# Optimization experiments

Measured on AMD Instinct MI355X. Metric: run time of the kernel, lower is better.

The kernel has to match this reference:

```python
import jax, jax.numpy as jnp
import numpy as np


def _proj_prelu(x, W, b, a):
    # 1x1 conv (pointwise linear over channels) + PReLU with scalar slope
    y = jnp.einsum('nchw,oc->nohw', x, W) + b[None, :, None, None]
    return jnp.where(y >= 0, y, a[0] * y)


def setup_inputs() -> dict:
    key = jax.random.key(0)
    ks = jax.random.split(key, 8)
    C, Ce = 128, 64
    x = jax.random.normal(ks[0], (4, C, 80, 80), dtype=jnp.float32)
    s = 1.0 / np.sqrt(C)
    Wq = jax.random.normal(ks[1], (Ce, C), dtype=jnp.float32) * s
    bq = jax.random.normal(ks[2], (Ce,), dtype=jnp.float32) * 0.01
    Wk = jax.random.normal(ks[3], (Ce, C), dtype=jnp.float32) * s
    bk = jax.random.normal(ks[4], (Ce,), dtype=jnp.float32) * 0.01
    Wv = jax.random.normal(ks[5], (C, C), dtype=jnp.float32) * s
    bv = jax.random.normal(ks[6], (C,), dtype=jnp.float32) * 0.01
    aq = jnp.full((1,), 0.25, dtype=jnp.float32)
    ak = jnp.full((1,), 0.25, dtype=jnp.float32)
    av = jnp.full((1,), 0.25, dtype=jnp.float32)
    return {'x': x, 'Wq': Wq, 'bq': bq, 'aq': aq, 'Wk': Wk, 'bk': bk,
            'ak': ak, 'Wv': Wv, 'bv': bv, 'av': av}


def reference(x, Wq, bq, aq, Wk, bk, ak, Wv, bv, av):
    q = _proj_prelu(x, Wq, bq, aq)   # [N, Ce, H, W]
    k = _proj_prelu(x, Wk, bk, ak)   # [N, Ce, H, W]
    v = _proj_prelu(x, Wv, bv, av)   # [N, C,  H, W]
    N, Ce, H, W = q.shape
    Cv = v.shape[1]
    HW = H * W
    qf = q.reshape(N, Ce, HW)        # torch permute+view -> [N, HW, Ce] = qf^T
    kf = k.reshape(N, Ce, HW)
    vf = v.reshape(N, Cv, HW)
    score = jnp.einsum('nci,ncj->nij', qf, kf)      # [N, HW, HW]
    attn = jax.nn.softmax(score, axis=2)
    out = jnp.einsum('nij,ncj->nci', attn, vf)      # [N, Cv, HW]
    return out.reshape(N, Cv, H, W)
```

## Files before the change

kernel.cpp:

```cpp
#include <hip/hip_runtime.h>

typedef __attribute__((ext_vector_type(8)))  short bf16x8;
typedef __attribute__((ext_vector_type(16))) float f32x16;
typedef unsigned int u32;
typedef unsigned short u16;

#define HW 6400
#define L2E 1.44269504088896f
#define DEFER_THR 8.0f

__device__ inline u16 f2bf(float f) {
    u32 u = __builtin_bit_cast(u32, f);
    u32 r = (u + 0x7fffu + ((u >> 16) & 1u)) >> 16;
    return (u16)r;
}
__device__ inline u32 cvt_pk_bf16(float lo, float hi) {
    u32 r;
    asm("v_cvt_pk_bf16_f32 %0, %1, %2" : "=v"(r) : "v"(lo), "v"(hi));
    return r;
}
__device__ inline void gload_lds16(const void* g, void* l) {
    __builtin_amdgcn_global_load_lds(
        (const __attribute__((address_space(1))) u32*)g,
        (__attribute__((address_space(3))) u32*)l, 16, 0, 0);
}

__global__ __launch_bounds__(256) void proj_kernel(
    const float* __restrict__ x,
    const float* __restrict__ Wq, const float* __restrict__ bq, const float* __restrict__ aq,
    const float* __restrict__ Wk, const float* __restrict__ bk, const float* __restrict__ ak,
    const float* __restrict__ Wv, const float* __restrict__ bv, const float* __restrict__ av,
    u16* __restrict__ QTc, u16* __restrict__ KT, u16* __restrict__ Vw)
{
    __shared__ char xs[64 * 272];
    __shared__ char ktr[64 * 144];

    const int tid  = threadIdx.x;
    const int lane = tid & 63;
    const int w    = tid >> 6;
    const int l31  = lane & 31;
    const int h    = lane >> 5;

    const int blk = blockIdx.x;
    const int n   = blk / 100;
    const int pt  = blk - n * 100;
    const int p0  = pt * 64;

    const float* xb = x + (size_t)n * 128 * HW + p0;
    #pragma unroll
    for (int it = 0; it < 8; ++it) {
        int idx = it * 256 + tid;
        int c = idx >> 4, p4 = (idx & 15) * 4;
        float4 d = *(const float4*)(xb + (size_t)c * HW + p4);
        *(u16*)(xs + (p4 + 0) * 272 + c * 2) = f2bf(d.x);
        *(u16*)(xs + (p4 + 1) * 272 + c * 2) = f2bf(d.y);
        *(u16*)(xs + (p4 + 2) * 272 + c * 2) = f2bf(d.z);
        *(u16*)(xs + (p4 + 3) * 272 + c * 2) = f2bf(d.w);
    }
    __syncthreads();

    const float* Wsrc; const float* bsrc; float slope; float osc = 1.0f;
    if (w == 0)      { Wsrc = Wq;                 bsrc = bq;             slope = aq[0]; osc = L2E; }
    else if (w == 1) { Wsrc = Wk;                 bsrc = bk;             slope = ak[0]; }
    else             { Wsrc = Wv + (w-2)*64*128;  bsrc = bv + (w-2)*64;  slope = av[0]; }

    bf16x8 wf[2][8];
    #pragma unroll
    for (int cb = 0; cb < 2; ++cb)
        #pragma unroll
        for (int kc = 0; kc < 8; ++kc) {
            const float* ws = Wsrc + (cb * 32 + l31) * 128 + kc * 16 + h * 8;
            float4 a = *(const float4*)ws;
            float4 b = *(const float4*)(ws + 4);
            union { u32 u[4]; bf16x8 v; } uu;
            uu.u[0] = cvt_pk_bf16(a.x, a.y);
            uu.u[1] = cvt_pk_bf16(a.z, a.w);
            uu.u[2] = cvt_pk_bf16(b.x, b.y);
            uu.u[3] = cvt_pk_bf16(b.z, b.w);
            wf[cb][kc] = uu.v;
        }

    f32x16 acc[2][2] = {};
    #pragma unroll
    for (int kc = 0; kc < 8; ++kc) {
        bf16x8 xb0 = *(const bf16x8*)(xs + (l31)      * 272 + kc * 32 + h * 16);
        bf16x8 xb1 = *(const bf16x8*)(xs + (l31 + 32) * 272 + kc * 32 + h * 16);
        acc[0][0] = __builtin_amdgcn_mfma_f32_32x32x16_bf16(wf[0][kc], xb0, acc[0][0], 0, 0, 0);
        acc[0][1] = __builtin_amdgcn_mfma_f32_32x32x16_bf16(wf[0][kc], xb1, acc[0][1], 0, 0, 0);
        acc[1][0] = __builtin_amdgcn_mfma_f32_32x32x16_bf16(wf[1][kc], xb0, acc[1][0], 0, 0, 0);
        acc[1][1] = __builtin_amdgcn_mfma_f32_32x32x16_bf16(wf[1][kc], xb1, acc[1][1], 0, 0, 0);
    }

    if (w != 1) {
        u16* dst = (w == 0) ? (QTc + (size_t)n * 64 * HW)
                            : (Vw + ((size_t)n * 128 + (size_t)(w - 2) * 64) * HW);
        #pragma unroll
        for (int cb = 0; cb < 2; ++cb)
            #pragma unroll
            for (int pb = 0; pb < 2; ++pb)
                #pragma unroll
                for (int r = 0; r < 16; ++r) {
                    int ch = cb * 32 + (r & 3) + 8 * (r >> 2) + 4 * h;
                    float y = acc[cb][pb][r] + bsrc[ch];
                    y = (y >= 0.f) ? y : slope * y;
                    dst[(size_t)ch * HW + p0 + pb * 32 + l31] = f2bf(y * osc);
                }
    } else {
        #pragma unroll
        for (int cb = 0; cb < 2; ++cb)
            #pragma unroll
            for (int pb = 0; pb < 2; ++pb)
                #pragma unroll
                for (int rp = 0; rp < 8; ++rp) {
                    int r0 = rp * 2;
                    int ch = cb * 32 + (r0 & 3) + 8 * (r0 >> 2) + 4 * h;
                    float y0 = acc[cb][pb][r0]     + bsrc[ch];
                    float y1 = acc[cb][pb][r0 + 1] + bsrc[ch + 1];
                    y0 = (y0 >= 0.f) ? y0 : slope * y0;
                    y1 = (y1 >= 0.f) ? y1 : slope * y1;
                    *(u32*)(ktr + (pb * 32 + l31) * 144 + ch * 2) = cvt_pk_bf16(y0, y1);
                }
        #pragma unroll
        for (int i8 = 0; i8 < 8; ++i8) {
            int p = i8 * 8 + (lane >> 3);
            bf16x8 d = *(const bf16x8*)(ktr + p * 144 + (lane & 7) * 16);
            *(bf16x8*)(KT + ((size_t)n * HW + p0 + p) * 64 + (lane & 7) * 8) = d;
        }
    }
}

__global__ __launch_bounds__(256, 3) void attn_kernel(
    const u16* __restrict__ QTc, const u16* __restrict__ KT, const u16* __restrict__ Vw,
    float* __restrict__ out,
    float* __restrict__ Opart, float* __restrict__ Mpart, float* __restrict__ Lpart,
    int jsplit, int NT)
{
    __shared__ char lds[49152];

    const int tid  = threadIdx.x;
    const int lane = tid & 63;
    const int w    = tid >> 6;
    const int l31  = lane & 31;
    const int h    = lane >> 5;

    const int per_n = 50 * jsplit;
    const int n    = blockIdx.x / per_n;
    const int rem  = blockIdx.x - n * per_n;
    const int it   = rem / jsplit;
    const int js   = rem - it * jsplit;
    const int i0   = it * 128;
    const int jt0  = js * NT;

    const int row = i0 + w * 32 + l31;

    const u16* qb = QTc + (size_t)n * 64 * HW + row;
    bf16x8 qf[4];
    #pragma unroll
    for (int kc = 0; kc < 4; ++kc) {
        union { u16 s[8]; bf16x8 v; } uu;
        #pragma unroll
        for (int e = 0; e < 8; ++e)
            uu.s[e] = qb[(size_t)(kc * 16 + h * 8 + e) * HW];
        qf[kc] = uu.v;
    }

    const char* Kg = (const char*)(KT + (size_t)n * HW * 64);
    const char* Vg = (const char*)(Vw + (size_t)n * 128 * HW);

    auto stage = [&](int buf, int jt) {
        char* B = lds + buf * 24576;
        #pragma unroll
        for (int q = 0; q < 2; ++q) {
            int abase = (2 * w + q) * 1024;
            int a = abase + lane * 16;
            int r = a >> 7;
            gload_lds16(Kg + (size_t)jt * 8192 + (size_t)(a ^ ((r & 7) << 4)), B + abase);
        }
        #pragma unroll
        for (int q = 0; q < 4; ++q) {
            int abase = (4 * w + q) * 1024;
            int a = abase + lane * 16;
            int c = a >> 7, off = a & 127;
            gload_lds16(Vg + (size_t)c * 12800 + (size_t)jt * 128 + (size_t)(off ^ ((c & 7) << 4)),
                        B + 8192 + abase);
        }
    };

    f32x16 o_acc[4] = {};
    float m = -3e38f, lsum = 0.f;

    auto compute = [&](int buf) {
        char* Klds = lds + buf * 24576;
        char* Vlds = Klds + 8192;

        f32x16 s0 = {}, s1 = {};
        #pragma unroll
        for (int kc = 0; kc < 4; ++kc) {
            const int cidx = (2 * kc + h) * 16;
            bf16x8 kf0 = *(const bf16x8*)(Klds + l31 * 128        + (cidx ^ ((l31 & 7) << 4)));
            bf16x8 kf1 = *(const bf16x8*)(Klds + (32 + l31) * 128 + (cidx ^ ((l31 & 7) << 4)));
            s0 = __builtin_amdgcn_mfma_f32_32x32x16_bf16(kf0, qf[kc], s0, 0, 0, 0);
            s1 = __builtin_amdgcn_mfma_f32_32x32x16_bf16(kf1, qf[kc], s1, 0, 0, 0);
        }

        float rmax = s0[0];
        #pragma unroll
        for (int r = 1; r < 16; ++r) rmax = fmaxf(rmax, s0[r]);
        #pragma unroll
        for (int r = 0; r < 16; ++r) rmax = fmaxf(rmax, s1[r]);
        rmax = fmaxf(rmax, __shfl_xor(rmax, 32, 64));

        if (__any(rmax > m + DEFER_THR)) {
            float mnew = fmaxf(m, rmax);
            float alpha = exp2f(m - mnew);
            lsum *= alpha;
            #pragma unroll
            for (int cb = 0; cb < 4; ++cb)
                #pragma unroll
                for (int r = 0; r < 16; ++r) o_acc[cb][r] *= alpha;
            m = mnew;
        }

        float rs = 0.f;
        #pragma unroll
        for (int r = 0; r < 16; ++r) { s0[r] = exp2f(s0[r] - m); rs += s0[r]; }
        #pragma unroll
        for (int r = 0; r < 16; ++r) { s1[r] = exp2f(s1[r] - m); rs += s1[r]; }
        rs += __shfl_xor(rs, 32, 64);
        lsum += rs;

        bf16x8 pf[4];
        #pragma unroll
        for (int kb = 0; kb < 4; ++kb) {
            f32x16 sv = (kb < 2) ? s0 : s1;
            const int b = (kb & 1) * 8;
            u32 w0 = cvt_pk_bf16(sv[b + 0], sv[b + 1]);
            u32 w1 = cvt_pk_bf16(sv[b + 2], sv[b + 3]);
            u32 w2 = cvt_pk_bf16(sv[b + 4], sv[b + 5]);
            u32 w3 = cvt_pk_bf16(sv[b + 6], sv[b + 7]);
            asm("v_permlane32_swap_b32 %0, %1" : "+v"(w0), "+v"(w2));
            asm("v_permlane32_swap_b32 %0, %1" : "+v"(w1), "+v"(w3));
            union { u32 u[4]; bf16x8 v; } uu;
            uu.u[0] = w0; uu.u[1] = w1; uu.u[2] = w2; uu.u[3] = w3;
            pf[kb] = uu.v;
        }

        #pragma unroll
        for (int kb = 0; kb < 4; ++kb) {
            const int jidx = (2 * kb + h) * 16;
            #pragma unroll
            for (int cb = 0; cb < 4; ++cb) {
                const int crow = cb * 32 + l31;
                bf16x8 vf = *(const bf16x8*)(Vlds + crow * 128 + (jidx ^ ((crow & 7) << 4)));
                o_acc[cb] = __builtin_amdgcn_mfma_f32_32x32x16_bf16(vf, pf[kb], o_acc[cb], 0, 0, 0);
            }
        }
    };

    stage(0, jt0);
    __syncthreads();
    int t = 0;
    for (; t + 2 <= NT; t += 2) {
        stage(1, jt0 + t + 1);
        compute(0);
        __syncthreads();
        if (t + 2 < NT) stage(0, jt0 + t + 2);
        compute(1);
        __syncthreads();
    }
    if (t < NT) compute(0);

    if (Opart != nullptr) {
        float* Ob = Opart + (size_t)(js * 4 + n) * 128 * HW + row;
        #pragma unroll
        for (int cb = 0; cb < 4; ++cb)
            #pragma unroll
            for (int r = 0; r < 16; ++r) {
                int c = cb * 32 + (r & 3) + 8 * (r >> 2) + 4 * h;
                Ob[(size_t)c * HW] = o_acc[cb][r];
            }
        if (h == 0) {
            Mpart[(size_t)(js * 4 + n) * HW + row] = m;
            Lpart[(size_t)(js * 4 + n) * HW + row] = lsum;
        }
    } else {
        float inv = 1.f / lsum;
        float* ob = out + (size_t)n * 128 * HW + row;
        #pragma unroll
        for (int cb = 0; cb < 4; ++cb)
            #pragma unroll
            for (int r = 0; r < 16; ++r) {
                int c = cb * 32 + (r & 3) + 8 * (r >> 2) + 4 * h;
                ob[(size_t)c * HW] = o_acc[cb][r] * inv;
            }
    }
}

__global__ __launch_bounds__(256) void combine_kernel(
    const float* __restrict__ Opart, const float* __restrict__ Mpart,
    const float* __restrict__ Lpart, float* __restrict__ out)
{
    const int b = blockIdx.x;
    const int n = b / 100;
    const int rem = b - n * 100;
    const int cq = rem / 25;
    const int ic = rem - cq * 25;
    const int i = ic * 256 + threadIdx.x;

    float mj[4], wj[4];
    #pragma unroll
    for (int js = 0; js < 4; ++js) mj[js] = Mpart[(size_t)(js * 4 + n) * HW + i];
    float M = fmaxf(fmaxf(mj[0], mj[1]), fmaxf(mj[2], mj[3]));
    float L = 0.f;
    #pragma unroll
    for (int js = 0; js < 4; ++js) {
        wj[js] = exp2f(mj[js] - M);
        L += Lpart[(size_t)(js * 4 + n) * HW + i] * wj[js];
    }
    const float inv = 1.f / L;

    for (int c = cq * 32; c < cq * 32 + 32; ++c) {
        float acc = 0.f;
        #pragma unroll
        for (int js = 0; js < 4; ++js)
            acc += Opart[((size_t)(js * 4 + n) * 128 + c) * HW + i] * wj[js];
        out[((size_t)n * 128 + c) * HW + i] = acc * inv;
    }
}

extern "C" void kernel_launch(void* const* d_in, const int* in_sizes, int n_in,
                              void* d_out, int out_size, void* d_ws, size_t ws_size,
                              hipStream_t stream) {
    const float* x  = (const float*)d_in[0];
    const float* Wq = (const float*)d_in[1];
    const float* bq = (const float*)d_in[2];
    const float* aq = (const float*)d_in[3];
    const float* Wk = (const float*)d_in[4];
    const float* bk = (const float*)d_in[5];
    const float* ak = (const float*)d_in[6];
    const float* Wv = (const float*)d_in[7];
    const float* bv = (const float*)d_in[8];
    const float* av = (const float*)d_in[9];

    char* wsp = (char*)d_ws;
    u16* QTc = (u16*)wsp;
    u16* KT  = (u16*)(wsp + 3276800);
    u16* Vw  = (u16*)(wsp + 6553600);
    const size_t base = 13107200;
    float* Opart = (float*)(wsp + base);
    float* Mpart = (float*)(wsp + base + 52428800);
    float* Lpart = (float*)(wsp + base + 52428800 + 409600);
    const size_t need = base + 52428800 + 2 * 409600;

    proj_kernel<<<dim3(400), 256, 0, stream>>>(x, Wq, bq, aq, Wk, bk, ak, Wv, bv, av,
                                               QTc, KT, Vw);

    if (ws_size >= need) {
        attn_kernel<<<dim3(4 * 50 * 4), 256, 0, stream>>>(QTc, KT, Vw, (float*)d_out,
                                                          Opart, Mpart, Lpart, 4, 25);
        combine_kernel<<<dim3(400), 256, 0, stream>>>(Opart, Mpart, Lpart, (float*)d_out);
    } else {
        attn_kernel<<<dim3(200), 256, 0, stream>>>(QTc, KT, Vw, (float*)d_out,
                                                   nullptr, nullptr, nullptr, 1, 100);
    }
}
```

Baseline: 134.1 us.

## Process two query row tiles per wave to reuse K/V fragments, split keys five ways

Each wave now handles 64 query rows (two 32-row tiles) instead of 32, so every K and V fragment read from LDS feeds two MFMAs. This halves LDS traffic per unit of work and improves the MFMA-to-load ratio. The LDS layout changes from XOR-swizzled rows to a chunk-major layout, and the row-sum reduction across half-waves moves to the end of the loop. The key dimension is split up to 5 ways when the workspace allows, to keep enough blocks in flight. The costs are higher register pressure (occupancy hint lowered to 2) and a possible LDS bank-conflict change from the new layout.

```diff
diff --git a/kernel.cpp b/kernel.cpp
--- a/kernel.cpp
+++ b/kernel.cpp
@@ -129,7 +129,7 @@
     }
 }
 
-__global__ __launch_bounds__(256, 3) void attn_kernel(
+__global__ __launch_bounds__(256, 2) void attn_kernel(
     const u16* __restrict__ QTc, const u16* __restrict__ KT, const u16* __restrict__ Vw,
     float* __restrict__ out,
     float* __restrict__ Opart, float* __restrict__ Mpart, float* __restrict__ Lpart,
@@ -143,25 +143,29 @@
     const int l31  = lane & 31;
     const int h    = lane >> 5;
 
-    const int per_n = 50 * jsplit;
+    const int per_n = 25 * jsplit;
     const int n    = blockIdx.x / per_n;
     const int rem  = blockIdx.x - n * per_n;
     const int it   = rem / jsplit;
     const int js   = rem - it * jsplit;
-    const int i0   = it * 128;
+    const int i0   = it * 256;
     const int jt0  = js * NT;
 
-    const int row = i0 + w * 32 + l31;
-
-    const u16* qb = QTc + (size_t)n * 64 * HW + row;
-    bf16x8 qf[4];
+    const int rowA = i0 + w * 64 + l31;
+    const int rowB = rowA + 32;
+
+    const u16* qbA = QTc + (size_t)n * 64 * HW + rowA;
+    bf16x8 qfA[4], qfB[4];
     #pragma unroll
     for (int kc = 0; kc < 4; ++kc) {
-        union { u16 s[8]; bf16x8 v; } uu;
-        #pragma unroll
-        for (int e = 0; e < 8; ++e)
-            uu.s[e] = qb[(size_t)(kc * 16 + h * 8 + e) * HW];
-        qf[kc] = uu.v;
+        union { u16 s[8]; bf16x8 v; } ua, ub;
+        #pragma unroll
+        for (int e = 0; e < 8; ++e) {
+            size_t off = (size_t)(kc * 16 + h * 8 + e) * HW;
+            ua.s[e] = qbA[off];
+            ub.s[e] = qbA[off + 32];
+        }
+        qfA[kc] = ua.v; qfB[kc] = ub.v;
     }
 
     const char* Kg = (const char*)(KT + (size_t)n * HW * 64);
@@ -171,88 +175,103 @@
         char* B = lds + buf * 24576;
         #pragma unroll
         for (int q = 0; q < 2; ++q) {
-            int abase = (2 * w + q) * 1024;
-            int a = abase + lane * 16;
-            int r = a >> 7;
-            gload_lds16(Kg + (size_t)jt * 8192 + (size_t)(a ^ ((r & 7) << 4)), B + abase);
+            int cc = w + 4 * q;
+            gload_lds16(Kg + (size_t)jt * 8192 + lane * 128 + cc * 16, B + cc * 1024);
         }
         #pragma unroll
         for (int q = 0; q < 4; ++q) {
-            int abase = (4 * w + q) * 1024;
-            int a = abase + lane * 16;
-            int c = a >> 7, off = a & 127;
-            gload_lds16(Vg + (size_t)c * 12800 + (size_t)jt * 128 + (size_t)(off ^ ((c & 7) << 4)),
-                        B + 8192 + abase);
+            int v = w + 4 * q;
+            int jcc = v >> 1, chalf = v & 1;
+            gload_lds16(Vg + (size_t)(chalf * 64 + lane) * 12800 + (size_t)jt * 128 + jcc * 16,
+                        B + 8192 + v * 1024);
         }
     };
 
-    f32x16 o_acc[4] = {};
-    float m = -3e38f, lsum = 0.f;
+    f32x16 accA[4] = {}, accB[4] = {};
+    float mA = -3e38f, mB = -3e38f, lsA = 0.f, lsB = 0.f;
 
     auto compute = [&](int buf) {
         char* Klds = lds + buf * 24576;
         char* Vlds = Klds + 8192;
 
-        f32x16 s0 = {}, s1 = {};
-        #pragma unroll
-        for (int kc = 0; kc < 4; ++kc) {
-            const int cidx = (2 * kc + h) * 16;
-            bf16x8 kf0 = *(const bf16x8*)(Klds + l31 * 128        + (cidx ^ ((l31 & 7) << 4)));
-            bf16x8 kf1 = *(const bf16x8*)(Klds + (32 + l31) * 128 + (cidx ^ ((l31 & 7) << 4)));
-            s0 = __builtin_amdgcn_mfma_f32_32x32x16_bf16(kf0, qf[kc], s0, 0, 0, 0);
-            s1 = __builtin_amdgcn_mfma_f32_32x32x16_bf16(kf1, qf[kc], s1, 0, 0, 0);
-        }
-
-        float rmax = s0[0];
-        #pragma unroll
-        for (int r = 1; r < 16; ++r) rmax = fmaxf(rmax, s0[r]);
-        #pragma unroll
-        for (int r = 0; r < 16; ++r) rmax = fmaxf(rmax, s1[r]);
-        rmax = fmaxf(rmax, __shfl_xor(rmax, 32, 64));
-
-        if (__any(rmax > m + DEFER_THR)) {
-            float mnew = fmaxf(m, rmax);
-            float alpha = exp2f(m - mnew);
-            lsum *= alpha;
-            #pragma unroll
-            for (int cb = 0; cb < 4; ++cb)
+        #pragma unroll
+        for (int jb = 0; jb < 2; ++jb) {
+            bf16x8 kf[4];
+            #pragma unroll
+            for (int kc = 0; kc < 4; ++kc)
+                kf[kc] = *(const bf16x8*)(Klds + (2 * kc + h) * 1024 + (jb * 32 + l31) * 16);
+
+            f32x16 sA = {}, sB = {};
+            #pragma unroll
+            for (int kc = 0; kc < 4; ++kc) {
+                sA = __builtin_amdgcn_mfma_f32_32x32x16_bf16(kf[kc], qfA[kc], sA, 0, 0, 0);
+                sB = __builtin_amdgcn_mfma_f32_32x32x16_bf16(kf[kc], qfB[kc], sB, 0, 0, 0);
+            }
+
+            float rmxA = sA[0], rmxB = sB[0];
+            #pragma unroll
+            for (int r = 1; r < 16; ++r) {
+                rmxA = fmaxf(rmxA, sA[r]);
+                rmxB = fmaxf(rmxB, sB[r]);
+            }
+            rmxA = fmaxf(rmxA, __shfl_xor(rmxA, 32, 64));
+            rmxB = fmaxf(rmxB, __shfl_xor(rmxB, 32, 64));
+
+            if (__any(rmxA > mA + DEFER_THR) || __any(rmxB > mB + DEFER_THR)) {
+                float mnA = fmaxf(mA, rmxA), mnB = fmaxf(mB, rmxB);
+                float aA = exp2f(mA - mnA), aB = exp2f(mB - mnB);
+                lsA *= aA; lsB *= aB;
                 #pragma unroll
-                for (int r = 0; r < 16; ++r) o_acc[cb][r] *= alpha;
-            m = mnew;
-        }
-
-        float rs = 0.f;
-        #pragma unroll
-        for (int r = 0; r < 16; ++r) { s0[r] = exp2f(s0[r] - m); rs += s0[r]; }
-        #pragma unroll
-        for (int r = 0; r < 16; ++r) { s1[r] = exp2f(s1[r] - m); rs += s1[r]; }
-        rs += __shfl_xor(rs, 32, 64);
-        lsum += rs;
-
-        bf16x8 pf[4];
-        #pragma unroll
-        for (int kb = 0; kb < 4; ++kb) {
-            f32x16 sv = (kb < 2) ? s0 : s1;
-            const int b = (kb & 1) * 8;
-            u32 w0 = cvt_pk_bf16(sv[b + 0], sv[b + 1]);
-            u32 w1 = cvt_pk_bf16(sv[b + 2], sv[b + 3]);
-            u32 w2 = cvt_pk_bf16(sv[b + 4], sv[b + 5]);
-            u32 w3 = cvt_pk_bf16(sv[b + 6], sv[b + 7]);
-            asm("v_permlane32_swap_b32 %0, %1" : "+v"(w0), "+v"(w2));
-            asm("v_permlane32_swap_b32 %0, %1" : "+v"(w1), "+v"(w3));
-            union { u32 u[4]; bf16x8 v; } uu;
-            uu.u[0] = w0; uu.u[1] = w1; uu.u[2] = w2; uu.u[3] = w3;
-            pf[kb] = uu.v;
-        }
-
-        #pragma unroll
-        for (int kb = 0; kb < 4; ++kb) {
-            const int jidx = (2 * kb + h) * 16;
-            #pragma unroll
-            for (int cb = 0; cb < 4; ++cb) {
-                const int crow = cb * 32 + l31;
-                bf16x8 vf = *(const bf16x8*)(Vlds + crow * 128 + (jidx ^ ((crow & 7) << 4)));
-                o_acc[cb] = __builtin_amdgcn_mfma_f32_32x32x16_bf16(vf, pf[kb], o_acc[cb], 0, 0, 0);
+                for (int cb = 0; cb < 4; ++cb)
+                    #pragma unroll
+                    for (int r = 0; r < 16; ++r) {
+                        accA[cb][r] *= aA;
+                        accB[cb][r] *= aB;
+                    }
+                mA = mnA; mB = mnB;
+            }
+
+            float rsA = 0.f, rsB = 0.f;
+            #pragma unroll
+            for (int r = 0; r < 16; ++r) {
+                sA[r] = exp2f(sA[r] - mA); rsA += sA[r];
+                sB[r] = exp2f(sB[r] - mB); rsB += sB[r];
+            }
+            lsA += rsA; lsB += rsB;
+
+            bf16x8 pfA[2], pfB[2];
+            #pragma unroll
+            for (int kbl = 0; kbl < 2; ++kbl) {
+                const int b = kbl * 8;
+                u32 a0 = cvt_pk_bf16(sA[b + 0], sA[b + 1]);
+                u32 a1 = cvt_pk_bf16(sA[b + 2], sA[b + 3]);
+                u32 a2 = cvt_pk_bf16(sA[b + 4], sA[b + 5]);
+                u32 a3 = cvt_pk_bf16(sA[b + 6], sA[b + 7]);
+                asm("v_permlane32_swap_b32 %0, %1" : "+v"(a0), "+v"(a2));
+                asm("v_permlane32_swap_b32 %0, %1" : "+v"(a1), "+v"(a3));
+                union { u32 u[4]; bf16x8 v; } ua;
+                ua.u[0] = a0; ua.u[1] = a1; ua.u[2] = a2; ua.u[3] = a3;
+                pfA[kbl] = ua.v;
+                u32 b0 = cvt_pk_bf16(sB[b + 0], sB[b + 1]);
+                u32 b1 = cvt_pk_bf16(sB[b + 2], sB[b + 3]);
+                u32 b2 = cvt_pk_bf16(sB[b + 4], sB[b + 5]);
+                u32 b3 = cvt_pk_bf16(sB[b + 6], sB[b + 7]);
+                asm("v_permlane32_swap_b32 %0, %1" : "+v"(b0), "+v"(b2));
+                asm("v_permlane32_swap_b32 %0, %1" : "+v"(b1), "+v"(b3));
+                union { u32 u[4]; bf16x8 v; } ub;
+                ub.u[0] = b0; ub.u[1] = b1; ub.u[2] = b2; ub.u[3] = b3;
+                pfB[kbl] = ub.v;
+            }
+
+            #pragma unroll
+            for (int kbl = 0; kbl < 2; ++kbl) {
+                const int jcc = jb * 4 + 2 * kbl + h;
+                #pragma unroll
+                for (int cb = 0; cb < 4; ++cb) {
+                    bf16x8 vf = *(const bf16x8*)(Vlds + jcc * 2048 + (cb * 32 + l31) * 16);
+                    accA[cb] = __builtin_amdgcn_mfma_f32_32x32x16_bf16(vf, pfA[kbl], accA[cb], 0, 0, 0);
+                    accB[cb] = __builtin_amdgcn_mfma_f32_32x32x16_bf16(vf, pfB[kbl], accB[cb], 0, 0, 0);
+                }
             }
         }
     };
@@ -270,35 +289,42 @@
     }
     if (t < NT) compute(0);
 
+    lsA += __shfl_xor(lsA, 32, 64);
+    lsB += __shfl_xor(lsB, 32, 64);
+
     if (Opart != nullptr) {
-        float* Ob = Opart + (size_t)(js * 4 + n) * 128 * HW + row;
+        float* Ob = Opart + (size_t)(js * 4 + n) * 128 * HW;
         #pragma unroll
         for (int cb = 0; cb < 4; ++cb)
             #pragma unroll
             for (int r = 0; r < 16; ++r) {
                 int c = cb * 32 + (r & 3) + 8 * (r >> 2) + 4 * h;
-                Ob[(size_t)c * HW] = o_acc[cb][r];
+                Ob[(size_t)c * HW + rowA] = accA[cb][r];
+                Ob[(size_t)c * HW + rowB] = accB[cb][r];
             }
         if (h == 0) {
-            Mpart[(size_t)(js * 4 + n) * HW + row] = m;
-            Lpart[(size_t)(js * 4 + n) * HW + row] = lsum;
+            Mpart[(size_t)(js * 4 + n) * HW + rowA] = mA;
+            Mpart[(size_t)(js * 4 + n) * HW + rowB] = mB;
+            Lpart[(size_t)(js * 4 + n) * HW + rowA] = lsA;
+            Lpart[(size_t)(js * 4 + n) * HW + rowB] = lsB;
         }
     } else {
-        float inv = 1.f / lsum;
-        float* ob = out + (size_t)n * 128 * HW + row;
+        float invA = 1.f / lsA, invB = 1.f / lsB;
+        float* ob = out + (size_t)n * 128 * HW;
         #pragma unroll
         for (int cb = 0; cb < 4; ++cb)
             #pragma unroll
             for (int r = 0; r < 16; ++r) {
                 int c = cb * 32 + (r & 3) + 8 * (r >> 2) + 4 * h;
-                ob[(size_t)c * HW] = o_acc[cb][r] * inv;
+                ob[(size_t)c * HW + rowA] = accA[cb][r] * invA;
+                ob[(size_t)c * HW + rowB] = accB[cb][r] * invB;
             }
     }
 }
 
 __global__ __launch_bounds__(256) void combine_kernel(
     const float* __restrict__ Opart, const float* __restrict__ Mpart,
-    const float* __restrict__ Lpart, float* __restrict__ out)
+    const float* __restrict__ Lpart, float* __restrict__ out, int jsplit)
 {
     const int b = blockIdx.x;
     const int n = b / 100;
@@ -307,23 +333,27 @@
     const int ic = rem - cq * 25;
     const int i = ic * 256 + threadIdx.x;
 
-    float mj[4], wj[4];
-    #pragma unroll
-    for (int js = 0; js < 4; ++js) mj[js] = Mpart[(size_t)(js * 4 + n) * HW + i];
-    float M = fmaxf(fmaxf(mj[0], mj[1]), fmaxf(mj[2], mj[3]));
+    float mj[5], wj[5];
+    float M = -3e38f;
+    #pragma unroll
+    for (int js = 0; js < 5; ++js) {
+        mj[js] = (js < jsplit) ? Mpart[(size_t)(js * 4 + n) * HW + i] : -3e38f;
+        M = fmaxf(M, mj[js]);
+    }
     float L = 0.f;
     #pragma unroll
-    for (int js = 0; js < 4; ++js) {
-        wj[js] = exp2f(mj[js] - M);
-        L += Lpart[(size_t)(js * 4 + n) * HW + i] * wj[js];
+    for (int js = 0; js < 5; ++js) {
+        wj[js] = (js < jsplit) ? exp2f(mj[js] - M) : 0.f;
+        if (js < jsplit) L += Lpart[(size_t)(js * 4 + n) * HW + i] * wj[js];
     }
     const float inv = 1.f / L;
 
     for (int c = cq * 32; c < cq * 32 + 32; ++c) {
         float acc = 0.f;
         #pragma unroll
-        for (int js = 0; js < 4; ++js)
-            acc += Opart[((size_t)(js * 4 + n) * 128 + c) * HW + i] * wj[js];
+        for (int js = 0; js < 5; ++js)
+            if (js < jsplit)
+                acc += Opart[((size_t)(js * 4 + n) * 128 + c) * HW + i] * wj[js];
         out[((size_t)n * 128 + c) * HW + i] = acc * inv;
     }
 }
@@ -347,20 +377,28 @@
     u16* KT  = (u16*)(wsp + 3276800);
     u16* Vw  = (u16*)(wsp + 6553600);
     const size_t base = 13107200;
-    float* Opart = (float*)(wsp + base);
-    float* Mpart = (float*)(wsp + base + 52428800);
-    float* Lpart = (float*)(wsp + base + 52428800 + 409600);
-    const size_t need = base + 52428800 + 2 * 409600;
+    const size_t oslab = 13107200;
+    const size_t mslab = 102400;
 
     proj_kernel<<<dim3(400), 256, 0, stream>>>(x, Wq, bq, aq, Wk, bk, ak, Wv, bv, av,
                                                QTc, KT, Vw);
 
-    if (ws_size >= need) {
-        attn_kernel<<<dim3(4 * 50 * 4), 256, 0, stream>>>(QTc, KT, Vw, (float*)d_out,
-                                                          Opart, Mpart, Lpart, 4, 25);
-        combine_kernel<<<dim3(400), 256, 0, stream>>>(Opart, Mpart, Lpart, (float*)d_out);
+    int jsplit = 0;
+    for (int js = 5; js >= 4; --js) {
+        size_t need = base + (size_t)js * (oslab + 2 * mslab);
+        if (ws_size >= need) { jsplit = js; break; }
+    }
+
+    if (jsplit > 0) {
+        float* Opart = (float*)(wsp + base);
+        float* Mpart = (float*)(wsp + base + (size_t)jsplit * oslab);
+        float* Lpart = (float*)(wsp + base + (size_t)jsplit * (oslab + mslab));
+        int NT = 100 / jsplit;
+        attn_kernel<<<dim3(4 * 25 * jsplit), 256, 0, stream>>>(QTc, KT, Vw, (float*)d_out,
+                                                               Opart, Mpart, Lpart, jsplit, NT);
+        combine_kernel<<<dim3(400), 256, 0, stream>>>(Opart, Mpart, Lpart, (float*)d_out, jsplit);
     } else {
-        attn_kernel<<<dim3(200), 256, 0, stream>>>(QTc, KT, Vw, (float*)d_out,
+        attn_kernel<<<dim3(100), 256, 0, stream>>>(QTc, KT, Vw, (float*)d_out,
                                                    nullptr, nullptr, nullptr, 1, 100);
     }
 }
```

Result: slower. 172.0 us (+28.2%).
